# Performance work log

Hardware: AMD Instinct MI355X
Metric: run time of the kernel (lower is better)

## Reference

```python
import jax, jax.numpy as jnp
import numpy as np

N_CLASSES = 64
NUM_PROPAGATIONS = 3
TEMPERATURE = 1.0
IN_FEAT = 512
EMB_DIM = 128
N_SUPPORT = 3200
N_QUERY = 200000


def _cdist(a, b):
    # Euclidean distance [N, C] without materializing [N, C, D]
    a2 = jnp.sum(a * a, axis=-1, keepdims=True)          # [N, 1]
    b2 = jnp.sum(b * b, axis=-1)[None, :]                # [1, C]
    d2 = a2 + b2 - 2.0 * (a @ b.T)
    return jnp.sqrt(jnp.maximum(d2, 0.0))


def setup_inputs() -> dict:
    key = jax.random.key(0)
    k1, k2, k3, k4 = jax.random.split(key, 4)
    support = jax.random.normal(k1, (1, N_SUPPORT, IN_FEAT), dtype=jnp.float32)
    query = jax.random.normal(k2, (1, N_QUERY, IN_FEAT), dtype=jnp.float32)
    support_labels = (jnp.arange(N_SUPPORT, dtype=jnp.int32) % N_CLASSES)
    # encoder: Linear(IN_FEAT -> EMB_DIM)
    W = jax.random.normal(k3, (IN_FEAT, EMB_DIM), dtype=jnp.float32) * 0.05
    b = jax.random.normal(k4, (EMB_DIM,), dtype=jnp.float32) * 0.05
    return {"support": support, "query": query, "support_labels": support_labels,
            "W": W, "b": b}


def reference(support, query, support_labels, W, b):
    s_emb = support[0] @ W + b            # [Ns, D]
    q_emb = query[0] @ W + b              # [Nq, D]
    all_emb = jnp.concatenate([s_emb, q_emb], axis=0)   # [N, D]
    n_total = all_emb.shape[0]

    # initial prototypes: per-class mean of support embeddings (segment mean)
    sums = jax.ops.segment_sum(s_emb, support_labels, num_segments=N_CLASSES)
    counts = jax.ops.segment_sum(jnp.ones((s_emb.shape[0],), s_emb.dtype),
                                 support_labels, num_segments=N_CLASSES)
    prototypes = sums / jnp.maximum(counts, 1.0)[:, None]   # [C, D]

    attn = jax.nn.softmax(-_cdist(all_emb, prototypes) / TEMPERATURE, axis=-1)  # [N, C]
    for _ in range(NUM_PROPAGATIONS):
        # attention-weighted mean prototype: mean_n attn[n, c] * emb[n]
        prototypes = (attn.T @ all_emb) / n_total            # [C, D]
        attn = jax.nn.softmax(-_cdist(all_emb, prototypes) / TEMPERATURE, axis=-1)

    logits = -_cdist(q_emb, prototypes) / TEMPERATURE        # [Nq, C]
    return logits[None]                                      # [1, Nq, C]
```

## Files before the change

### kernel.cpp

```cpp
#include <hip/hip_runtime.h>

#define NS 3200
#define NQ 200000
#define NTOT (NS + NQ)
#define KIN 512
#define ED 128
#define NC 64
#define INV_N (1.0f / (float)NTOT)

typedef short short8 __attribute__((ext_vector_type(8)));
typedef short short4v __attribute__((ext_vector_type(4)));
typedef float floatx4 __attribute__((ext_vector_type(4)));

static __device__ __forceinline__ unsigned short f2bf(float f) {
    unsigned int u = __float_as_uint(f);
    u += 0x7FFF + ((u >> 16) & 1);
    return (unsigned short)(u >> 16);
}
static __device__ __forceinline__ float bf2f(unsigned short h) {
    return __uint_as_float(((unsigned int)h) << 16);
}

__global__ __launch_bounds__(256) void prep_wt(const float* __restrict__ W,
                                               unsigned short* __restrict__ WT)
{
    int idx = blockIdx.x * 256 + threadIdx.x;
#pragma unroll
    for (int p = 0; p < 4; ++p) {
        int id = idx + p * 16384;
        int n = id >> 9, k = id & 511;
        WT[n * 512 + k] = f2bf(W[k * 128 + n]);
    }
}

__global__ __launch_bounds__(256) void encode_mfma(
    const float* __restrict__ X, const unsigned short* __restrict__ WT,
    const float* __restrict__ bias, unsigned short* __restrict__ emb,
    float* __restrict__ en2)
{
    __shared__ unsigned short Xs[64 * 72];
    __shared__ unsigned short Ws[128 * 72];

    const int t = threadIdx.x;
    const int w = t >> 6;
    const int lane = t & 63;
    const int q = lane >> 4;
    const int i = lane & 15;
    const long row0 = (long)blockIdx.x * 64;

    floatx4 acc[8];
#pragma unroll
    for (int ct = 0; ct < 8; ++ct) acc[ct] = (floatx4){0.f, 0.f, 0.f, 0.f};

    for (int kk0 = 0; kk0 < KIN; kk0 += 64) {
#pragma unroll
        for (int p = 0; p < 4; ++p) {
            int id = p * 256 + t;
            int r = id >> 4, kf4 = id & 15;
            float4 v = *(const float4*)&X[(row0 + r) * KIN + kk0 + kf4 * 4];
            short4v h;
            h[0] = (short)f2bf(v.x); h[1] = (short)f2bf(v.y);
            h[2] = (short)f2bf(v.z); h[3] = (short)f2bf(v.w);
            *(short4v*)&Xs[r * 72 + kf4 * 4] = h;
        }
#pragma unroll
        for (int p = 0; p < 4; ++p) {
            int id = p * 256 + t;
            int n = id >> 3, ch = id & 7;
            uint4 v = *(const uint4*)&WT[n * 512 + kk0 + ch * 8];
            *(uint4*)&Ws[n * 72 + ch * 8] = v;
        }
        __syncthreads();
#pragma unroll
        for (int ks = 0; ks < 2; ++ks) {
            short8 a = *(const short8*)&Xs[(w * 16 + i) * 72 + ks * 32 + q * 8];
#pragma unroll
            for (int ct = 0; ct < 8; ++ct) {
                short8 b = *(const short8*)&Ws[(ct * 16 + i) * 72 + ks * 32 + q * 8];
                acc[ct] = __builtin_amdgcn_mfma_f32_16x16x32_bf16(a, b, acc[ct], 0, 0, 0);
            }
        }
        __syncthreads();
    }

    float sq[4] = {0.f, 0.f, 0.f, 0.f};
#pragma unroll
    for (int ct = 0; ct < 8; ++ct) {
        float bb = bias[ct * 16 + i];
#pragma unroll
        for (int r = 0; r < 4; ++r) {
            float v = acc[ct][r] + bb;
            long row = row0 + w * 16 + q * 4 + r;
            emb[row * ED + ct * 16 + i] = f2bf(v);
            sq[r] += v * v;
        }
    }
#pragma unroll
    for (int r = 0; r < 4; ++r) {
        float s = sq[r];
        s += __shfl_xor(s, 1); s += __shfl_xor(s, 2);
        s += __shfl_xor(s, 4); s += __shfl_xor(s, 8);
        if (i == 0) en2[row0 + w * 16 + q * 4 + r] = s;
    }
}

__global__ __launch_bounds__(128) void proto_init(
    const unsigned short* __restrict__ emb, const int* __restrict__ labels,
    float* __restrict__ proto)
{
    const int c = blockIdx.x, d = threadIdx.x;
    float acc = 0.f; int cnt = 0;
    for (int r4 = 0; r4 < NS; r4 += 4) {
        int4 lb = *(const int4*)&labels[r4];
        if (lb.x == c) { acc += bf2f(emb[(r4 + 0) * ED + d]); cnt++; }
        if (lb.y == c) { acc += bf2f(emb[(r4 + 1) * ED + d]); cnt++; }
        if (lb.z == c) { acc += bf2f(emb[(r4 + 2) * ED + d]); cnt++; }
        if (lb.w == c) { acc += bf2f(emb[(r4 + 3) * ED + d]); cnt++; }
    }
    proto[c * ED + d] = acc / fmaxf((float)cnt, 1.0f);
}

__global__ __launch_bounds__(256) void propagate(
    const unsigned short* __restrict__ emb, const float* __restrict__ en2,
    const float* __restrict__ proto_src, float scale,
    float* __restrict__ accum)
{
    __shared__ unsigned short Pbf[64 * 136];
    __shared__ unsigned short ET[128 * 66];
    __shared__ unsigned short ScT[64 * 72];
    __shared__ float pn2s[64];

    const int t = threadIdx.x;
    const int w = t >> 6, lane = t & 63, q = lane >> 4, i = lane & 15;

    {
        int c = t >> 2, part = t & 3;
        const float* src = &proto_src[c * 128 + part * 32];
        float sqv = 0.f;
#pragma unroll 8
        for (int j = 0; j < 32; ++j) {
            float v = src[j] * scale;
            Pbf[c * 136 + part * 32 + j] = f2bf(v);
            sqv += v * v;
        }
        sqv += __shfl_xor(sqv, 1);
        sqv += __shfl_xor(sqv, 2);
        if (part == 0) pn2s[c] = sqv;
    }
    __syncthreads();

    short8 bP[4][4];
#pragma unroll
    for (int ct = 0; ct < 4; ++ct)
#pragma unroll
        for (int ks = 0; ks < 4; ++ks)
            bP[ct][ks] = *(const short8*)&Pbf[(ct * 16 + i) * 136 + ks * 32 + q * 8];
    float pn[4];
#pragma unroll
    for (int ct = 0; ct < 4; ++ct) pn[ct] = pn2s[ct * 16 + i];

    floatx4 acc2[8];
#pragma unroll
    for (int nt = 0; nt < 8; ++nt) acc2[nt] = (floatx4){0.f, 0.f, 0.f, 0.f};

    const int ntiles = NTOT / 64;
    for (int tile = blockIdx.x; tile < ntiles; tile += gridDim.x) {
        const long row0 = (long)tile * 64;

        short8 aE[4];
#pragma unroll
        for (int ks = 0; ks < 4; ++ks)
            aE[ks] = *(const short8*)&emb[(row0 + w * 16 + i) * ED + ks * 32 + q * 8];
        float en[4];
#pragma unroll
        for (int r = 0; r < 4; ++r) en[r] = en2[row0 + w * 16 + q * 4 + r];

#pragma unroll
        for (int ks = 0; ks < 4; ++ks)
#pragma unroll
            for (int j = 0; j < 8; ++j)
                ET[(ks * 32 + q * 8 + j) * 66 + w * 16 + i] = (unsigned short)aE[ks][j];

        floatx4 s1[4];
#pragma unroll
        for (int ct = 0; ct < 4; ++ct) s1[ct] = (floatx4){0.f, 0.f, 0.f, 0.f};
#pragma unroll
        for (int ks = 0; ks < 4; ++ks)
#pragma unroll
            for (int ct = 0; ct < 4; ++ct)
                s1[ct] = __builtin_amdgcn_mfma_f32_16x16x32_bf16(aE[ks], bP[ct][ks], s1[ct], 0, 0, 0);

        float attn[4][4];
#pragma unroll
        for (int r = 0; r < 4; ++r) {
            float sc[4];
#pragma unroll
            for (int ct = 0; ct < 4; ++ct) {
                float d2 = en[r] + pn[ct] - 2.f * s1[ct][r];
                sc[ct] = -sqrtf(fmaxf(d2, 0.f));
            }
            float mx = fmaxf(fmaxf(sc[0], sc[1]), fmaxf(sc[2], sc[3]));
            mx = fmaxf(mx, __shfl_xor(mx, 1));
            mx = fmaxf(mx, __shfl_xor(mx, 2));
            mx = fmaxf(mx, __shfl_xor(mx, 4));
            mx = fmaxf(mx, __shfl_xor(mx, 8));
            float sm = 0.f;
#pragma unroll
            for (int ct = 0; ct < 4; ++ct) { attn[ct][r] = __expf(sc[ct] - mx); sm += attn[ct][r]; }
            sm += __shfl_xor(sm, 1);
            sm += __shfl_xor(sm, 2);
            sm += __shfl_xor(sm, 4);
            sm += __shfl_xor(sm, 8);
            float inv = 1.f / sm;
#pragma unroll
            for (int ct = 0; ct < 4; ++ct) attn[ct][r] *= inv;
        }
#pragma unroll
        for (int ct = 0; ct < 4; ++ct) {
            short4v pk;
            pk[0] = (short)f2bf(attn[ct][0]); pk[1] = (short)f2bf(attn[ct][1]);
            pk[2] = (short)f2bf(attn[ct][2]); pk[3] = (short)f2bf(attn[ct][3]);
            *(short4v*)&ScT[(ct * 16 + i) * 72 + w * 16 + q * 4] = pk;
        }
        __syncthreads();

#pragma unroll
        for (int ks2 = 0; ks2 < 2; ++ks2) {
            short8 a2 = *(const short8*)&ScT[(w * 16 + i) * 72 + ks2 * 32 + q * 8];
#pragma unroll
            for (int nt = 0; nt < 8; ++nt) {
                union { short8 s; unsigned int u[4]; } b2;
                const unsigned short* base = &ET[(nt * 16 + i) * 66 + ks2 * 32 + q * 8];
                b2.u[0] = *(const unsigned int*)&base[0];
                b2.u[1] = *(const unsigned int*)&base[2];
                b2.u[2] = *(const unsigned int*)&base[4];
                b2.u[3] = *(const unsigned int*)&base[6];
                acc2[nt] = __builtin_amdgcn_mfma_f32_16x16x32_bf16(a2, b2.s, acc2[nt], 0, 0, 0);
            }
        }
        __syncthreads();
    }

#pragma unroll
    for (int nt = 0; nt < 8; ++nt)
#pragma unroll
        for (int r = 0; r < 4; ++r)
            atomicAdd(&accum[(w * 16 + q * 4 + r) * ED + nt * 16 + i], acc2[nt][r]);
}

__global__ __launch_bounds__(256) void logits_k(
    const unsigned short* __restrict__ emb, const float* __restrict__ en2,
    const float* __restrict__ proto_src, float scale, float* __restrict__ out)
{
    __shared__ unsigned short Pbf[64 * 136];
    __shared__ float pn2s[64];

    const int t = threadIdx.x;
    const int w = t >> 6, lane = t & 63, q = lane >> 4, i = lane & 15;

    {
        int c = t >> 2, part = t & 3;
        const float* src = &proto_src[c * 128 + part * 32];
        float sqv = 0.f;
#pragma unroll 8
        for (int j = 0; j < 32; ++j) {
            float v = src[j] * scale;
            Pbf[c * 136 + part * 32 + j] = f2bf(v);
            sqv += v * v;
        }
        sqv += __shfl_xor(sqv, 1);
        sqv += __shfl_xor(sqv, 2);
        if (part == 0) pn2s[c] = sqv;
    }
    __syncthreads();

    short8 bP[4][4];
#pragma unroll
    for (int ct = 0; ct < 4; ++ct)
#pragma unroll
        for (int ks = 0; ks < 4; ++ks)
            bP[ct][ks] = *(const short8*)&Pbf[(ct * 16 + i) * 136 + ks * 32 + q * 8];
    float pn[4];
#pragma unroll
    for (int ct = 0; ct < 4; ++ct) pn[ct] = pn2s[ct * 16 + i];

    const int ntiles = NQ / 64;
    for (int tile = blockIdx.x; tile < ntiles; tile += gridDim.x) {
        const long row0 = (long)tile * 64;

        short8 aE[4];
#pragma unroll
        for (int ks = 0; ks < 4; ++ks)
            aE[ks] = *(const short8*)&emb[(row0 + w * 16 + i) * ED + ks * 32 + q * 8];
        float en[4];
#pragma unroll
        for (int r = 0; r < 4; ++r) en[r] = en2[row0 + w * 16 + q * 4 + r];

        floatx4 s1[4];
#pragma unroll
        for (int ct = 0; ct < 4; ++ct) s1[ct] = (floatx4){0.f, 0.f, 0.f, 0.f};
#pragma unroll
        for (int ks = 0; ks < 4; ++ks)
#pragma unroll
            for (int ct = 0; ct < 4; ++ct)
                s1[ct] = __builtin_amdgcn_mfma_f32_16x16x32_bf16(aE[ks], bP[ct][ks], s1[ct], 0, 0, 0);

#pragma unroll
        for (int r = 0; r < 4; ++r) {
            long row = row0 + w * 16 + q * 4 + r;
#pragma unroll
            for (int ct = 0; ct < 4; ++ct) {
                float d2 = en[r] + pn[ct] - 2.f * s1[ct][r];
                out[row * NC + ct * 16 + i] = -sqrtf(fmaxf(d2, 0.f));
            }
        }
    }
}

extern "C" void kernel_launch(void* const* d_in, const int* in_sizes, int n_in,
                              void* d_out, int out_size, void* d_ws, size_t ws_size,
                              hipStream_t stream)
{
    (void)in_sizes; (void)n_in; (void)out_size; (void)ws_size;

    const float* support = (const float*)d_in[0];
    const float* query   = (const float*)d_in[1];
    const int*   labels  = (const int*)d_in[2];
    const float* W       = (const float*)d_in[3];
    const float* bias    = (const float*)d_in[4];
    float* out = (float*)d_out;

    unsigned short* emb = (unsigned short*)d_ws;
    float* en2 = (float*)(emb + (size_t)NTOT * ED);
    unsigned short* WT = (unsigned short*)(en2 + NTOT);
    float* proto0 = (float*)(WT + 128 * 512);
    float* accA = proto0 + NC * ED;
    float* accB = accA + NC * ED;

    prep_wt<<<64, 256, 0, stream>>>(W, WT);
    encode_mfma<<<NS / 64, 256, 0, stream>>>(support, WT, bias, emb, en2);
    encode_mfma<<<NQ / 64, 256, 0, stream>>>(query, WT, bias,
                                             emb + (size_t)NS * ED, en2 + NS);
    proto_init<<<NC, ED, 0, stream>>>(emb, labels, proto0);

    hipMemsetAsync(accA, 0, NC * ED * sizeof(float), stream);
    propagate<<<512, 256, 0, stream>>>(emb, en2, proto0, 1.0f, accA);

    hipMemsetAsync(accB, 0, NC * ED * sizeof(float), stream);
    propagate<<<512, 256, 0, stream>>>(emb, en2, accA, INV_N, accB);

    hipMemsetAsync(accA, 0, NC * ED * sizeof(float), stream);
    propagate<<<512, 256, 0, stream>>>(emb, en2, accB, INV_N, accA);

    logits_k<<<1024, 256, 0, stream>>>(emb + (size_t)NS * ED, en2 + NS,
                                       accA, INV_N, out);
}
```

Before: 891.8 us.

## Drop LDS staging in encoder and replace atomic prototype reduction with partials

```diff
diff --git a/kernel.cpp b/kernel.cpp
--- a/kernel.cpp
+++ b/kernel.cpp
@@ -7,6 +7,7 @@
 #define ED 128
 #define NC 64
 #define INV_N (1.0f / (float)NTOT)
+#define PGRID 512
 
 typedef short short8 __attribute__((ext_vector_type(8)));
 typedef short short4v __attribute__((ext_vector_type(4)));
@@ -33,75 +34,79 @@
     }
 }
 
-__global__ __launch_bounds__(256) void encode_mfma(
+__global__ __launch_bounds__(512) void encode_mfma(
     const float* __restrict__ X, const unsigned short* __restrict__ WT,
     const float* __restrict__ bias, unsigned short* __restrict__ emb,
-    float* __restrict__ en2)
-{
-    __shared__ unsigned short Xs[64 * 72];
-    __shared__ unsigned short Ws[128 * 72];
-
+    float* __restrict__ en2, int nrows)
+{
     const int t = threadIdx.x;
-    const int w = t >> 6;
-    const int lane = t & 63;
-    const int q = lane >> 4;
-    const int i = lane & 15;
-    const long row0 = (long)blockIdx.x * 64;
-
-    floatx4 acc[8];
-#pragma unroll
-    for (int ct = 0; ct < 8; ++ct) acc[ct] = (floatx4){0.f, 0.f, 0.f, 0.f};
-
-    for (int kk0 = 0; kk0 < KIN; kk0 += 64) {
-#pragma unroll
-        for (int p = 0; p < 4; ++p) {
-            int id = p * 256 + t;
-            int r = id >> 4, kf4 = id & 15;
-            float4 v = *(const float4*)&X[(row0 + r) * KIN + kk0 + kf4 * 4];
-            short4v h;
-            h[0] = (short)f2bf(v.x); h[1] = (short)f2bf(v.y);
-            h[2] = (short)f2bf(v.z); h[3] = (short)f2bf(v.w);
-            *(short4v*)&Xs[r * 72 + kf4 * 4] = h;
-        }
-#pragma unroll
-        for (int p = 0; p < 4; ++p) {
-            int id = p * 256 + t;
-            int n = id >> 3, ch = id & 7;
-            uint4 v = *(const uint4*)&WT[n * 512 + kk0 + ch * 8];
-            *(uint4*)&Ws[n * 72 + ch * 8] = v;
-        }
-        __syncthreads();
-#pragma unroll
-        for (int ks = 0; ks < 2; ++ks) {
-            short8 a = *(const short8*)&Xs[(w * 16 + i) * 72 + ks * 32 + q * 8];
-#pragma unroll
-            for (int ct = 0; ct < 8; ++ct) {
-                short8 b = *(const short8*)&Ws[(ct * 16 + i) * 72 + ks * 32 + q * 8];
-                acc[ct] = __builtin_amdgcn_mfma_f32_16x16x32_bf16(a, b, acc[ct], 0, 0, 0);
-            }
-        }
-        __syncthreads();
-    }
-
-    float sq[4] = {0.f, 0.f, 0.f, 0.f};
+    const int w = t >> 6, lane = t & 63, q = lane >> 4, i = lane & 15;
+    const long row0 = (long)blockIdx.x * 256;
+
+    long xr0 = row0 + w * 32 + i;
+    long xr1 = xr0 + 16;
+    if (xr0 > nrows - 1) xr0 = nrows - 1;
+    if (xr1 > nrows - 1) xr1 = nrows - 1;
+    const float* xp0 = &X[xr0 * KIN + q * 8];
+    const float* xp1 = &X[xr1 * KIN + q * 8];
+    const unsigned short* wp = &WT[(long)i * 512 + q * 8];
+
+    floatx4 acc0[8], acc1[8];
 #pragma unroll
     for (int ct = 0; ct < 8; ++ct) {
-        float bb = bias[ct * 16 + i];
-#pragma unroll
-        for (int r = 0; r < 4; ++r) {
-            float v = acc[ct][r] + bb;
-            long row = row0 + w * 16 + q * 4 + r;
-            emb[row * ED + ct * 16 + i] = f2bf(v);
-            sq[r] += v * v;
-        }
-    }
-#pragma unroll
-    for (int r = 0; r < 4; ++r) {
-        float s = sq[r];
-        s += __shfl_xor(s, 1); s += __shfl_xor(s, 2);
-        s += __shfl_xor(s, 4); s += __shfl_xor(s, 8);
-        if (i == 0) en2[row0 + w * 16 + q * 4 + r] = s;
-    }
+        acc0[ct] = (floatx4){0.f, 0.f, 0.f, 0.f};
+        acc1[ct] = (floatx4){0.f, 0.f, 0.f, 0.f};
+    }
+
+#pragma unroll
+    for (int kk = 0; kk < KIN; kk += 32) {
+        floatx4 f0a = *(const floatx4*)(xp0 + kk);
+        floatx4 f0b = *(const floatx4*)(xp0 + kk + 4);
+        floatx4 f1a = *(const floatx4*)(xp1 + kk);
+        floatx4 f1b = *(const floatx4*)(xp1 + kk + 4);
+        short8 a0, a1;
+        a0[0] = (short)f2bf(f0a[0]); a0[1] = (short)f2bf(f0a[1]);
+        a0[2] = (short)f2bf(f0a[2]); a0[3] = (short)f2bf(f0a[3]);
+        a0[4] = (short)f2bf(f0b[0]); a0[5] = (short)f2bf(f0b[1]);
+        a0[6] = (short)f2bf(f0b[2]); a0[7] = (short)f2bf(f0b[3]);
+        a1[0] = (short)f2bf(f1a[0]); a1[1] = (short)f2bf(f1a[1]);
+        a1[2] = (short)f2bf(f1a[2]); a1[3] = (short)f2bf(f1a[3]);
+        a1[4] = (short)f2bf(f1b[0]); a1[5] = (short)f2bf(f1b[1]);
+        a1[6] = (short)f2bf(f1b[2]); a1[7] = (short)f2bf(f1b[3]);
+#pragma unroll
+        for (int ct = 0; ct < 8; ++ct) {
+            short8 b = *(const short8*)&wp[ct * 16 * 512 + kk];
+            acc0[ct] = __builtin_amdgcn_mfma_f32_16x16x32_bf16(a0, b, acc0[ct], 0, 0, 0);
+            acc1[ct] = __builtin_amdgcn_mfma_f32_16x16x32_bf16(a1, b, acc1[ct], 0, 0, 0);
+        }
+    }
+
+    float bb[8];
+#pragma unroll
+    for (int ct = 0; ct < 8; ++ct) bb[ct] = bias[ct * 16 + i];
+
+#define EPILOGUE(ACC, RF)                                                      \
+    {                                                                          \
+        _Pragma("unroll")                                                      \
+        for (int r = 0; r < 4; ++r) {                                          \
+            long row = row0 + w * 32 + (RF) * 16 + q * 4 + r;                  \
+            bool ok = row < nrows;                                             \
+            float s = 0.f;                                                     \
+            _Pragma("unroll")                                                  \
+            for (int ct = 0; ct < 8; ++ct) {                                   \
+                float v = ACC[ct][r] + bb[ct];                                 \
+                if (ok) emb[row * ED + ct * 16 + i] = f2bf(v);                 \
+                s += v * v;                                                    \
+            }                                                                  \
+            s += __shfl_xor(s, 1); s += __shfl_xor(s, 2);                      \
+            s += __shfl_xor(s, 4); s += __shfl_xor(s, 8);                      \
+            if (ok && i == 0) en2[row] = s;                                    \
+        }                                                                      \
+    }
+
+    EPILOGUE(acc0, 0)
+    EPILOGUE(acc1, 1)
+#undef EPILOGUE
 }
 
 __global__ __launch_bounds__(128) void proto_init(
@@ -123,7 +128,7 @@
 __global__ __launch_bounds__(256) void propagate(
     const unsigned short* __restrict__ emb, const float* __restrict__ en2,
     const float* __restrict__ proto_src, float scale,
-    float* __restrict__ accum)
+    float* __restrict__ partial)
 {
     __shared__ unsigned short Pbf[64 * 136];
     __shared__ unsigned short ET[128 * 66];
@@ -241,11 +246,22 @@
         __syncthreads();
     }
 
+    float* myp = partial + (size_t)blockIdx.x * (NC * ED);
 #pragma unroll
     for (int nt = 0; nt < 8; ++nt)
 #pragma unroll
         for (int r = 0; r < 4; ++r)
-            atomicAdd(&accum[(w * 16 + q * 4 + r) * ED + nt * 16 + i], acc2[nt][r]);
+            myp[(w * 16 + q * 4 + r) * ED + nt * 16 + i] = acc2[nt][r];
+}
+
+__global__ __launch_bounds__(256) void reduce_partials(
+    const float* __restrict__ partial, float* __restrict__ proto)
+{
+    int idx = blockIdx.x * 256 + threadIdx.x;
+    float s = 0.f;
+#pragma unroll 8
+    for (int b = 0; b < PGRID; ++b) s += partial[(size_t)b * (NC * ED) + idx];
+    proto[idx] = s;
 }
 
 __global__ __launch_bounds__(256) void logits_k(
@@ -334,24 +350,25 @@
     float* en2 = (float*)(emb + (size_t)NTOT * ED);
     unsigned short* WT = (unsigned short*)(en2 + NTOT);
     float* proto0 = (float*)(WT + 128 * 512);
-    float* accA = proto0 + NC * ED;
-    float* accB = accA + NC * ED;
+    float* protoA = proto0 + NC * ED;
+    float* protoB = protoA + NC * ED;
+    float* part   = protoB + NC * ED;
 
     prep_wt<<<64, 256, 0, stream>>>(W, WT);
-    encode_mfma<<<NS / 64, 256, 0, stream>>>(support, WT, bias, emb, en2);
-    encode_mfma<<<NQ / 64, 256, 0, stream>>>(query, WT, bias,
-                                             emb + (size_t)NS * ED, en2 + NS);
+    encode_mfma<<<(NS + 255) / 256, 512, 0, stream>>>(support, WT, bias, emb, en2, NS);
+    encode_mfma<<<(NQ + 255) / 256, 512, 0, stream>>>(query, WT, bias,
+                                                      emb + (size_t)NS * ED, en2 + NS, NQ);
     proto_init<<<NC, ED, 0, stream>>>(emb, labels, proto0);
 
-    hipMemsetAsync(accA, 0, NC * ED * sizeof(float), stream);
-    propagate<<<512, 256, 0, stream>>>(emb, en2, proto0, 1.0f, accA);
-
-    hipMemsetAsync(accB, 0, NC * ED * sizeof(float), stream);
-    propagate<<<512, 256, 0, stream>>>(emb, en2, accA, INV_N, accB);
-
-    hipMemsetAsync(accA, 0, NC * ED * sizeof(float), stream);
-    propagate<<<512, 256, 0, stream>>>(emb, en2, accB, INV_N, accA);
+    propagate<<<PGRID, 256, 0, stream>>>(emb, en2, proto0, 1.0f, part);
+    reduce_partials<<<32, 256, 0, stream>>>(part, protoA);
+
+    propagate<<<PGRID, 256, 0, stream>>>(emb, en2, protoA, INV_N, part);
+    reduce_partials<<<32, 256, 0, stream>>>(part, protoB);
+
+    propagate<<<PGRID, 256, 0, stream>>>(emb, en2, protoB, INV_N, part);
+    reduce_partials<<<32, 256, 0, stream>>>(part, protoA);
 
     logits_k<<<1024, 256, 0, stream>>>(emb + (size_t)NS * ED, en2 + NS,
-                                       accA, INV_N, out);
-}
+                                       protoA, INV_N, out);
+}
```

After: 1.047 ms. 17.5% more time.

## Double-buffer encoder X tiles and replace propagate atomics with partial-sum reduction

Applied to the files above, without the earlier changes.

```diff
diff --git a/kernel.cpp b/kernel.cpp
--- a/kernel.cpp
+++ b/kernel.cpp
@@ -7,6 +7,7 @@
 #define ED 128
 #define NC 64
 #define INV_N (1.0f / (float)NTOT)
+#define PGRID 512
 
 typedef short short8 __attribute__((ext_vector_type(8)));
 typedef short short4v __attribute__((ext_vector_type(4)));
@@ -38,50 +39,59 @@
     const float* __restrict__ bias, unsigned short* __restrict__ emb,
     float* __restrict__ en2)
 {
-    __shared__ unsigned short Xs[64 * 72];
-    __shared__ unsigned short Ws[128 * 72];
+    __shared__ unsigned short Xs[2][64 * 72];
 
     const int t = threadIdx.x;
-    const int w = t >> 6;
-    const int lane = t & 63;
-    const int q = lane >> 4;
-    const int i = lane & 15;
+    const int w = t >> 6, lane = t & 63, q = lane >> 4, i = lane & 15;
     const long row0 = (long)blockIdx.x * 64;
 
+    const int sr = t >> 4;
+    const int skf = t & 15;
+    const float* xbase = &X[(row0 + sr) * KIN + skf * 4];
+
     floatx4 acc[8];
 #pragma unroll
     for (int ct = 0; ct < 8; ++ct) acc[ct] = (floatx4){0.f, 0.f, 0.f, 0.f};
 
-    for (int kk0 = 0; kk0 < KIN; kk0 += 64) {
-#pragma unroll
-        for (int p = 0; p < 4; ++p) {
-            int id = p * 256 + t;
-            int r = id >> 4, kf4 = id & 15;
-            float4 v = *(const float4*)&X[(row0 + r) * KIN + kk0 + kf4 * 4];
-            short4v h;
-            h[0] = (short)f2bf(v.x); h[1] = (short)f2bf(v.y);
-            h[2] = (short)f2bf(v.z); h[3] = (short)f2bf(v.w);
-            *(short4v*)&Xs[r * 72 + kf4 * 4] = h;
-        }
-#pragma unroll
-        for (int p = 0; p < 4; ++p) {
-            int id = p * 256 + t;
-            int n = id >> 3, ch = id & 7;
-            uint4 v = *(const uint4*)&WT[n * 512 + kk0 + ch * 8];
-            *(uint4*)&Ws[n * 72 + ch * 8] = v;
-        }
+    float4 L[4];
+#define STAGE_LOAD(S)                                                          \
+    {                                                                          \
+        _Pragma("unroll")                                                      \
+        for (int p = 0; p < 4; ++p)                                            \
+            L[p] = *(const float4*)&xbase[(long)p * 16 * KIN + (S) * 64];      \
+    }
+#define STAGE_WRITE(B)                                                         \
+    {                                                                          \
+        _Pragma("unroll")                                                      \
+        for (int p = 0; p < 4; ++p) {                                          \
+            short4v h;                                                         \
+            h[0] = (short)f2bf(L[p].x); h[1] = (short)f2bf(L[p].y);            \
+            h[2] = (short)f2bf(L[p].z); h[3] = (short)f2bf(L[p].w);            \
+            *(short4v*)&Xs[B][(sr + p * 16) * 72 + skf * 4] = h;               \
+        }                                                                      \
+    }
+
+    STAGE_LOAD(0)
+    STAGE_WRITE(0)
+
+#pragma unroll
+    for (int s = 0; s < 8; ++s) {
+        if (s < 7) STAGE_LOAD(s + 1)
         __syncthreads();
+        const unsigned short* xsb = &Xs[s & 1][0];
 #pragma unroll
         for (int ks = 0; ks < 2; ++ks) {
-            short8 a = *(const short8*)&Xs[(w * 16 + i) * 72 + ks * 32 + q * 8];
+            short8 a = *(const short8*)&xsb[(w * 16 + i) * 72 + ks * 32 + q * 8];
 #pragma unroll
             for (int ct = 0; ct < 8; ++ct) {
-                short8 b = *(const short8*)&Ws[(ct * 16 + i) * 72 + ks * 32 + q * 8];
+                short8 b = *(const short8*)&WT[(ct * 16 + i) * 512 + s * 64 + ks * 32 + q * 8];
                 acc[ct] = __builtin_amdgcn_mfma_f32_16x16x32_bf16(a, b, acc[ct], 0, 0, 0);
             }
         }
-        __syncthreads();
-    }
+        if (s < 7) STAGE_WRITE((s + 1) & 1)
+    }
+#undef STAGE_LOAD
+#undef STAGE_WRITE
 
     float sq[4] = {0.f, 0.f, 0.f, 0.f};
 #pragma unroll
@@ -123,7 +133,7 @@
 __global__ __launch_bounds__(256) void propagate(
     const unsigned short* __restrict__ emb, const float* __restrict__ en2,
     const float* __restrict__ proto_src, float scale,
-    float* __restrict__ accum)
+    float* __restrict__ partial)
 {
     __shared__ unsigned short Pbf[64 * 136];
     __shared__ unsigned short ET[128 * 66];
@@ -241,11 +251,22 @@
         __syncthreads();
     }
 
+    float* myp = partial + (size_t)blockIdx.x * (NC * ED);
 #pragma unroll
     for (int nt = 0; nt < 8; ++nt)
 #pragma unroll
         for (int r = 0; r < 4; ++r)
-            atomicAdd(&accum[(w * 16 + q * 4 + r) * ED + nt * 16 + i], acc2[nt][r]);
+            myp[(w * 16 + q * 4 + r) * ED + nt * 16 + i] = acc2[nt][r];
+}
+
+__global__ __launch_bounds__(256) void reduce_partials(
+    const float* __restrict__ partial, float* __restrict__ proto)
+{
+    int idx = blockIdx.x * 256 + threadIdx.x;
+    float s = 0.f;
+#pragma unroll 8
+    for (int b = 0; b < PGRID; ++b) s += partial[(size_t)b * (NC * ED) + idx];
+    proto[idx] = s;
 }
 
 __global__ __launch_bounds__(256) void logits_k(
@@ -334,8 +355,9 @@
     float* en2 = (float*)(emb + (size_t)NTOT * ED);
     unsigned short* WT = (unsigned short*)(en2 + NTOT);
     float* proto0 = (float*)(WT + 128 * 512);
-    float* accA = proto0 + NC * ED;
-    float* accB = accA + NC * ED;
+    float* protoA = proto0 + NC * ED;
+    float* protoB = protoA + NC * ED;
+    float* part   = protoB + NC * ED;
 
     prep_wt<<<64, 256, 0, stream>>>(W, WT);
     encode_mfma<<<NS / 64, 256, 0, stream>>>(support, WT, bias, emb, en2);
@@ -343,15 +365,15 @@
                                              emb + (size_t)NS * ED, en2 + NS);
     proto_init<<<NC, ED, 0, stream>>>(emb, labels, proto0);
 
-    hipMemsetAsync(accA, 0, NC * ED * sizeof(float), stream);
-    propagate<<<512, 256, 0, stream>>>(emb, en2, proto0, 1.0f, accA);
-
-    hipMemsetAsync(accB, 0, NC * ED * sizeof(float), stream);
-    propagate<<<512, 256, 0, stream>>>(emb, en2, accA, INV_N, accB);
-
-    hipMemsetAsync(accA, 0, NC * ED * sizeof(float), stream);
-    propagate<<<512, 256, 0, stream>>>(emb, en2, accB, INV_N, accA);
+    propagate<<<PGRID, 256, 0, stream>>>(emb, en2, proto0, 1.0f, part);
+    reduce_partials<<<32, 256, 0, stream>>>(part, protoA);
+
+    propagate<<<PGRID, 256, 0, stream>>>(emb, en2, protoA, INV_N, part);
+    reduce_partials<<<32, 256, 0, stream>>>(part, protoB);
+
+    propagate<<<PGRID, 256, 0, stream>>>(emb, en2, protoB, INV_N, part);
+    reduce_partials<<<32, 256, 0, stream>>>(part, protoA);
 
     logits_k<<<1024, 256, 0, stream>>>(emb + (size_t)NS * ED, en2 + NS,
-                                       accA, INV_N, out);
-}
+                                       protoA, INV_N, out);
+}
```

New measurement: 972.4 us. +9.0%, slower.
